# Kernel tuning notes

Measured on AMD Instinct MI355X. Metric: run time of the kernel, lower is better.

The kernel has to match this reference:

```python
import jax, jax.numpy as jnp
import numpy as np

B, L, T, D, H, DH = 8, 1024, 1024, 768, 12, 64
SPATIAL_DIM = 5


def setup_inputs() -> dict:
    key = jax.random.key(0)
    ks = jax.random.split(key, 12)
    scale = 1.0 / np.sqrt(D)
    inp = {
        "q": jax.random.normal(ks[0], (B, L, D), dtype=jnp.float32),
        "k": jax.random.normal(ks[1], (B, T, D), dtype=jnp.float32),
        "v": jax.random.normal(ks[2], (B, T, D), dtype=jnp.float32),
        "pairwise_locs": jax.random.normal(ks[3], (B, L, T, SPATIAL_DIM), dtype=jnp.float32),
        # last 64 key positions are padding in every batch row (never all-True)
        "key_padding_mask": jnp.broadcast_to(jnp.arange(T) >= T - 64, (B, T)),
        "Wq": jax.random.normal(ks[4], (D, H * DH), dtype=jnp.float32) * scale,
        "bq": jnp.zeros((H * DH,), dtype=jnp.float32),
        "Wk": jax.random.normal(ks[5], (D, H * DH), dtype=jnp.float32) * scale,
        "bk": jnp.zeros((H * DH,), dtype=jnp.float32),
        "Wv": jax.random.normal(ks[6], (D, H * DH), dtype=jnp.float32) * scale,
        "bv": jnp.zeros((H * DH,), dtype=jnp.float32),
        "Wo": jax.random.normal(ks[7], (H * DH, D), dtype=jnp.float32) * scale,
        "bo": jnp.zeros((D,), dtype=jnp.float32),
    }
    return inp


def reference(q, k, v, pairwise_locs, key_padding_mask, Wq, bq, Wk, bk, Wv, bv, Wo, bo):
    # pairwise_locs is accepted but unused in this forward path (as in the source).
    b, l, _ = q.shape
    t = k.shape[1]
    qh = (q @ Wq + bq).reshape(b, l, H, DH)  # b l h d
    kh = (k @ Wk + bk).reshape(b, t, H, DH)  # b t h d
    vh = (v @ Wv + bv).reshape(b, t, H, DH)  # b t h d
    attn = jnp.einsum('blhd,bthd->bhlt', qh, kh) / jnp.sqrt(jnp.float32(DH))
    attn = jnp.where(key_padding_mask[:, None, None, :], -jnp.inf, attn)
    fused_attn = jax.nn.softmax(attn, axis=-1)
    out = jnp.einsum('bhlt,bthd->blhd', fused_attn, vh).reshape(b, l, H * DH)
    return out @ Wo + bo  # dropout is identity in eval mode
```

## Files before the change

### kernel.cpp

```cpp
#include <hip/hip_runtime.h>
#include <hip/hip_bf16.h>
#include <cstdint>
#include <cstddef>

#define NB 8
#define NL 1024
#define NT 1024
#define ND 768
#define NH 12
#define NDH 64
#define NM (NB*NL)

typedef short short8 __attribute__((ext_vector_type(8)));
typedef unsigned short ushort4v __attribute__((ext_vector_type(4)));
typedef unsigned int uint4v __attribute__((ext_vector_type(4)));
typedef float f32x4 __attribute__((ext_vector_type(4)));
typedef float float4v __attribute__((ext_vector_type(4)));

__device__ __forceinline__ unsigned short f2bf(float f) {
  union { __hip_bfloat16 h; unsigned short u; } cv;
  cv.h = __float2bfloat16(f);
  return cv.u;
}
__device__ __forceinline__ unsigned pk2(float lo, float hi) {
  return (unsigned)f2bf(lo) | ((unsigned)f2bf(hi) << 16);
}
__device__ __forceinline__ void gll16(const void* g, void* l) {
  __builtin_amdgcn_global_load_lds(
      (const __attribute__((address_space(1))) unsigned int*)g,
      (__attribute__((address_space(3))) unsigned int*)l, 16, 0, 0);
}

__global__ __launch_bounds__(256) void wt_kernel(
    const float* __restrict__ W0, const float* __restrict__ W1,
    const float* __restrict__ W2, const float* __restrict__ W3,
    unsigned short* __restrict__ Wt) {
  __shared__ float tile[32][33];
  const float* W = blockIdx.z == 0 ? W0 : blockIdx.z == 1 ? W1 : blockIdx.z == 2 ? W2 : W3;
  const int k0 = blockIdx.x * 32, n0 = blockIdx.y * 32;
  const int tx = threadIdx.x & 31, ty = threadIdx.x >> 5;
  for (int r = ty; r < 32; r += 8) tile[r][tx] = W[(size_t)(k0 + r) * ND + n0 + tx];
  __syncthreads();
  unsigned short* out = Wt + (size_t)blockIdx.z * ND * ND;
  for (int r = ty; r < 32; r += 8) out[(size_t)(n0 + r) * ND + k0 + tx] = f2bf(tile[tx][r]);
}

template<int PROJ>
__global__ __launch_bounds__(256) void gemm_kernel(
    const float* __restrict__ qf, const float* __restrict__ kf,
    const float* __restrict__ vf, const unsigned short* __restrict__ aob,
    const unsigned short* __restrict__ Wt,
    const float* __restrict__ b0, const float* __restrict__ b1,
    const float* __restrict__ b2, const float* __restrict__ b3,
    unsigned short* __restrict__ qhb, unsigned short* __restrict__ khb,
    unsigned short* __restrict__ vhT, float* __restrict__ outf) {
  __shared__ __align__(16) unsigned short As[128 * 64];
  __shared__ __align__(16) unsigned short Bs[128 * 64];
  const int tid = threadIdx.x, lane = tid & 63, w = tid >> 6;
  const int c = lane & 15, g = lane >> 4;
  const int wrow = w & 1, wcol = w >> 1;
  const int l8 = lane >> 3, l7 = lane & 7, csw = l7 ^ l8;
  const int mbase = blockIdx.x * 128, nbase = blockIdx.y * 128;
  const int z = PROJ ? blockIdx.z : 3;

  const float* Af = PROJ ? (z == 0 ? qf : z == 1 ? kf : vf) : nullptr;
  const unsigned short* Bt = Wt + (size_t)z * ND * ND;
  const float* bias = z == 0 ? b0 : z == 1 ? b1 : z == 2 ? b2 : b3;

  f32x4 acc[4][4];
#pragma unroll
  for (int m = 0; m < 4; m++)
#pragma unroll
    for (int n = 0; n < 4; n++) acc[m][n] = (f32x4){0.f, 0.f, 0.f, 0.f};

  for (int k0 = 0; k0 < ND; k0 += 64) {
    if (PROJ) {
#pragma unroll
      for (int i = 0; i < 4; i++) {
        int id = i * 256 + tid;
        int r = id >> 3, cc = id & 7;
        const float* src = &Af[(size_t)(mbase + r) * ND + k0 + cc * 8];
        float4v x0 = *(const float4v*)src;
        float4v x1 = *(const float4v*)(src + 4);
        uint4v y = {pk2(x0[0], x0[1]), pk2(x0[2], x0[3]),
                    pk2(x1[0], x1[1]), pk2(x1[2], x1[3])};
        *(uint4v*)&As[r * 64 + ((cc ^ (r & 7)) * 8)] = y;
      }
    } else {
#pragma unroll
      for (int it = 0; it < 4; it++) {
        int r = it * 32 + w * 8 + l8;
        gll16(&aob[(size_t)(mbase + r) * ND + k0 + csw * 8],
              &As[(it * 32 + w * 8) * 64]);
      }
    }
#pragma unroll
    for (int it = 0; it < 4; it++) {
      int r = it * 32 + w * 8 + l8;
      gll16(&Bt[(size_t)(nbase + r) * ND + k0 + csw * 8],
            &Bs[(it * 32 + w * 8) * 64]);
    }
    __syncthreads();

#pragma unroll
    for (int ks = 0; ks < 2; ks++) {
      short8 a[4], b[4];
#pragma unroll
      for (int m = 0; m < 4; m++) {
        int r = wrow * 64 + m * 16 + c;
        a[m] = *(const short8*)&As[r * 64 + (((ks * 4 + g) ^ (c & 7)) * 8)];
      }
#pragma unroll
      for (int n = 0; n < 4; n++) {
        int r = wcol * 64 + n * 16 + c;
        b[n] = *(const short8*)&Bs[r * 64 + (((ks * 4 + g) ^ (c & 7)) * 8)];
      }
#pragma unroll
      for (int m = 0; m < 4; m++)
#pragma unroll
        for (int n = 0; n < 4; n++)
          acc[m][n] = __builtin_amdgcn_mfma_f32_16x16x32_bf16(a[m], b[n], acc[m][n], 0, 0, 0);
    }
    __syncthreads();
  }

#pragma unroll
  for (int n = 0; n < 4; n++) {
    const int col = nbase + wcol * 64 + n * 16 + c;
    const float bv = bias[col];
    if (!PROJ) {
#pragma unroll
      for (int m = 0; m < 4; m++) {
        const int r0 = mbase + wrow * 64 + m * 16 + g * 4;
#pragma unroll
        for (int j = 0; j < 4; j++)
          outf[(size_t)(r0 + j) * ND + col] = acc[m][n][j] + bv;
      }
    } else if (z == 2) {
      const int h = col >> 6, dd = col & 63;
#pragma unroll
      for (int m = 0; m < 4; m++) {
        const int r0 = mbase + wrow * 64 + m * 16 + g * 4;
        const int bb = r0 >> 10, t = r0 & (NT - 1);
        ushort4v y;
#pragma unroll
        for (int j = 0; j < 4; j++) y[j] = f2bf(acc[m][n][j] + bv);
        *(ushort4v*)&vhT[((size_t)(bb * NH + h) * NDH + dd) * NT + t] = y;
      }
    } else {
      unsigned short* outb = (z == 0) ? qhb : khb;
      const float scale = (z == 0) ? 0.125f : 1.0f;
#pragma unroll
      for (int m = 0; m < 4; m++) {
        const int r0 = mbase + wrow * 64 + m * 16 + g * 4;
#pragma unroll
        for (int j = 0; j < 4; j++)
          outb[(size_t)(r0 + j) * ND + col] = f2bf((acc[m][n][j] + bv) * scale);
      }
    }
  }
}

__global__ __launch_bounds__(256) void attn_kernel(
    const unsigned short* __restrict__ qh, const unsigned short* __restrict__ kh,
    const unsigned short* __restrict__ vhT, const unsigned int* __restrict__ mask,
    unsigned short* __restrict__ ao) {
  __shared__ __align__(16) unsigned short Ks[2][64 * 64];
  __shared__ __align__(16) unsigned short Vs[2][64 * 64];
  __shared__ __align__(16) unsigned short Ps[4][32][72];
  const int tid = threadIdx.x, lane = tid & 63, w = tid >> 6;
  const int c = lane & 15, g = lane >> 4;
  const int l8 = lane >> 3, l7 = lane & 7, csw = l7 ^ l8;
  const int qb = blockIdx.x * 128;
  const int b = blockIdx.y / NH, h = blockIdx.y % NH;
  const size_t kbase = (size_t)b * NT * ND + h * NDH;
  const size_t vbase = (size_t)(b * NH + h) * NDH * NT;

  short8 aq[2][2];
#pragma unroll
  for (int half = 0; half < 2; half++) {
    size_t qrow = (size_t)(b * NL + qb + w * 32 + half * 16 + c) * ND + h * NDH;
#pragma unroll
    for (int ks = 0; ks < 2; ks++)
      aq[half][ks] = *(const short8*)&qh[qrow + ks * 32 + g * 8];
  }

  f32x4 o[2][4];
#pragma unroll
  for (int half = 0; half < 2; half++)
#pragma unroll
    for (int f = 0; f < 4; f++) o[half][f] = (f32x4){0.f, 0.f, 0.f, 0.f};
  float mr[2] = {-1e30f, -1e30f}, lr[2] = {0.f, 0.f};

#pragma unroll
  for (int it = 0; it < 2; it++) {
    int r = w * 16 + it * 8 + l8;
    gll16(&kh[kbase + (size_t)r * ND + csw * 8], &Ks[0][(w * 16 + it * 8) * 64]);
    gll16(&vhT[vbase + (size_t)r * NT + csw * 8], &Vs[0][(w * 16 + it * 8) * 64]);
  }
  __syncthreads();

  for (int t0 = 0; t0 < NT; t0 += 64) {
    const int cur = (t0 >> 6) & 1;
    if (t0 + 64 < NT) {
#pragma unroll
      for (int it = 0; it < 2; it++) {
        int r = w * 16 + it * 8 + l8;
        gll16(&kh[kbase + (size_t)(t0 + 64 + r) * ND + csw * 8],
              &Ks[cur ^ 1][(w * 16 + it * 8) * 64]);
        gll16(&vhT[vbase + (size_t)r * NT + (t0 + 64) + csw * 8],
              &Vs[cur ^ 1][(w * 16 + it * 8) * 64]);
      }
    }

    f32x4 s[2][4];
#pragma unroll
    for (int half = 0; half < 2; half++)
#pragma unroll
      for (int n = 0; n < 4; n++) s[half][n] = (f32x4){0.f, 0.f, 0.f, 0.f};
#pragma unroll
    for (int ks = 0; ks < 2; ks++)
#pragma unroll
      for (int n = 0; n < 4; n++) {
        short8 ak = *(const short8*)&Ks[cur][(n * 16 + c) * 64 + (((ks * 4 + g) ^ (c & 7)) * 8)];
        s[0][n] = __builtin_amdgcn_mfma_f32_16x16x32_bf16(ak, aq[0][ks], s[0][n], 0, 0, 0);
        s[1][n] = __builtin_amdgcn_mfma_f32_16x16x32_bf16(ak, aq[1][ks], s[1][n], 0, 0, 0);
      }

#pragma unroll
    for (int n = 0; n < 4; n++) {
      uint4v mm = *(const uint4v*)&mask[(size_t)b * NT + t0 + n * 16 + g * 4];
#pragma unroll
      for (int j = 0; j < 4; j++)
        if (mm[j]) { s[0][n][j] = -INFINITY; s[1][n][j] = -INFINITY; }
    }

#pragma unroll
    for (int half = 0; half < 2; half++) {
      float m01 = fmaxf(fmaxf(s[half][0][0], s[half][0][1]), fmaxf(s[half][0][2], s[half][0][3]));
      float m23 = fmaxf(fmaxf(s[half][1][0], s[half][1][1]), fmaxf(s[half][1][2], s[half][1][3]));
      float m45 = fmaxf(fmaxf(s[half][2][0], s[half][2][1]), fmaxf(s[half][2][2], s[half][2][3]));
      float m67 = fmaxf(fmaxf(s[half][3][0], s[half][3][1]), fmaxf(s[half][3][2], s[half][3][3]));
      float mt = fmaxf(fmaxf(m01, m23), fmaxf(m45, m67));
      mt = fmaxf(mt, __shfl_xor(mt, 16, 64));
      mt = fmaxf(mt, __shfl_xor(mt, 32, 64));
      float mnew = fmaxf(mr[half], mt);
      float alpha = __expf(mr[half] - mnew);
      mr[half] = mnew;
      float rs = 0.f;
#pragma unroll
      for (int n = 0; n < 4; n++)
#pragma unroll
        for (int j = 0; j < 4; j++) {
          float p = __expf(s[half][n][j] - mnew);
          s[half][n][j] = p;
          rs += p;
        }
      rs += __shfl_xor(rs, 16, 64);
      rs += __shfl_xor(rs, 32, 64);
      lr[half] = lr[half] * alpha + rs;
#pragma unroll
      for (int f = 0; f < 4; f++)
#pragma unroll
        for (int j = 0; j < 4; j++) o[half][f][j] *= alpha;
      unsigned* pr = (unsigned*)&Ps[w][half * 16 + c][0];
#pragma unroll
      for (int n = 0; n < 4; n++) {
        pr[n * 8 + g * 2]     = pk2(s[half][n][0], s[half][n][1]);
        pr[n * 8 + g * 2 + 1] = pk2(s[half][n][2], s[half][n][3]);
      }
    }

#pragma unroll
    for (int ks = 0; ks < 2; ks++) {
      short8 bp0 = *(const short8*)&Ps[w][c][ks * 32 + g * 8];
      short8 bp1 = *(const short8*)&Ps[w][16 + c][ks * 32 + g * 8];
#pragma unroll
      for (int f = 0; f < 4; f++) {
        short8 av = *(const short8*)&Vs[cur][(f * 16 + c) * 64 + (((ks * 4 + g) ^ (c & 7)) * 8)];
        o[0][f] = __builtin_amdgcn_mfma_f32_16x16x32_bf16(av, bp0, o[0][f], 0, 0, 0);
        o[1][f] = __builtin_amdgcn_mfma_f32_16x16x32_bf16(av, bp1, o[1][f], 0, 0, 0);
      }
    }
    __syncthreads();
  }

#pragma unroll
  for (int half = 0; half < 2; half++) {
    float inv = 1.f / lr[half];
    size_t row = (size_t)(b * NL + qb + w * 32 + half * 16 + c) * ND + h * NDH;
#pragma unroll
    for (int f = 0; f < 4; f++) {
      ushort4v y;
#pragma unroll
      for (int j = 0; j < 4; j++) y[j] = f2bf(o[half][f][j] * inv);
      *(ushort4v*)&ao[row + f * 16 + g * 4] = y;
    }
  }
}

extern "C" void kernel_launch(void* const* d_in, const int* in_sizes, int n_in,
                              void* d_out, int out_size, void* d_ws, size_t ws_size,
                              hipStream_t stream) {
  const float* q  = (const float*)d_in[0];
  const float* k  = (const float*)d_in[1];
  const float* v  = (const float*)d_in[2];
  const unsigned int* mask = (const unsigned int*)d_in[4];
  const float* Wq = (const float*)d_in[5];
  const float* bq = (const float*)d_in[6];
  const float* Wk = (const float*)d_in[7];
  const float* bk = (const float*)d_in[8];
  const float* Wv = (const float*)d_in[9];
  const float* bv = (const float*)d_in[10];
  const float* Wo = (const float*)d_in[11];
  const float* bo = (const float*)d_in[12];
  float* out = (float*)d_out;

  unsigned short* ws  = (unsigned short*)d_ws;
  unsigned short* Wt  = ws;
  unsigned short* qhb = Wt + (size_t)4 * ND * ND;
  unsigned short* khb = qhb + (size_t)NM * ND;
  unsigned short* vhT = khb + (size_t)NM * ND;
  unsigned short* aob = vhT + (size_t)NM * ND;

  wt_kernel<<<dim3(ND / 32, ND / 32, 4), 256, 0, stream>>>(Wq, Wk, Wv, Wo, Wt);

  gemm_kernel<1><<<dim3(NM / 128, ND / 128, 3), 256, 0, stream>>>(
      q, k, v, nullptr, Wt, bq, bk, bv, bo, qhb, khb, vhT, nullptr);

  attn_kernel<<<dim3(NL / 128, NB * NH), 256, 0, stream>>>(qhb, khb, vhT, mask, aob);

  gemm_kernel<0><<<dim3(NM / 128, ND / 128, 1), 256, 0, stream>>>(
      nullptr, nullptr, nullptr, aob, Wt, bq, bk, bv, bo, nullptr, nullptr, nullptr, out);
}
```

Before: 160.6 us.

## Pre-convert inputs to bf16, vectorize GEMM epilogues, add lazy softmax rescale

Adds a separate kernel that converts q/k/v to bf16 up front, so every GEMM stages A through global_load_lds instead of doing per-tile fp32 loads and converts. The GEMM swaps MFMA operand order for non-V modes so each lane holds four consecutive columns, which allows vectorized bias loads and 4-wide stores. The V projection gets its own launch. In attention, the change adds s_setprio around the MFMA blocks, skips masking when a 64-key tile has no padded keys, and only rescales the running max and accumulators when the new max exceeds the old one by more than 8. The cost is an extra launch and an extra bf16 round trip through memory for the inputs. The lazy rescale trades strict max tracking for a bounded exp growth (up to e^8) in fp32.

```diff
diff --git a/kernel.cpp b/kernel.cpp
--- a/kernel.cpp
+++ b/kernel.cpp
@@ -29,6 +29,20 @@
   __builtin_amdgcn_global_load_lds(
       (const __attribute__((address_space(1))) unsigned int*)g,
       (__attribute__((address_space(3))) unsigned int*)l, 16, 0, 0);
+}
+
+__global__ __launch_bounds__(256) void cvt_kernel(
+    const float* __restrict__ q, const float* __restrict__ k,
+    const float* __restrict__ v, unsigned short* __restrict__ qb,
+    unsigned short* __restrict__ kb, unsigned short* __restrict__ vb) {
+  const float* src = blockIdx.y == 0 ? q : blockIdx.y == 1 ? k : v;
+  unsigned short* dst = blockIdx.y == 0 ? qb : blockIdx.y == 1 ? kb : vb;
+  size_t i = ((size_t)blockIdx.x * 256 + threadIdx.x) * 8;
+  float4v x0 = *(const float4v*)&src[i];
+  float4v x1 = *(const float4v*)&src[i + 4];
+  uint4v y = {pk2(x0[0], x0[1]), pk2(x0[2], x0[3]),
+              pk2(x1[0], x1[1]), pk2(x1[2], x1[3])};
+  *(uint4v*)&dst[i] = y;
 }
 
 __global__ __launch_bounds__(256) void wt_kernel(
@@ -45,15 +59,13 @@
   for (int r = ty; r < 32; r += 8) out[(size_t)(n0 + r) * ND + k0 + tx] = f2bf(tile[tx][r]);
 }
 
-template<int PROJ>
+template<int MODE>
 __global__ __launch_bounds__(256) void gemm_kernel(
-    const float* __restrict__ qf, const float* __restrict__ kf,
-    const float* __restrict__ vf, const unsigned short* __restrict__ aob,
+    const unsigned short* __restrict__ A0, const unsigned short* __restrict__ A1,
     const unsigned short* __restrict__ Wt,
-    const float* __restrict__ b0, const float* __restrict__ b1,
-    const float* __restrict__ b2, const float* __restrict__ b3,
-    unsigned short* __restrict__ qhb, unsigned short* __restrict__ khb,
-    unsigned short* __restrict__ vhT, float* __restrict__ outf) {
+    const float* __restrict__ bias0, const float* __restrict__ bias1,
+    unsigned short* __restrict__ outb0, unsigned short* __restrict__ outb1,
+    float* __restrict__ outf) {
   __shared__ __align__(16) unsigned short As[128 * 64];
   __shared__ __align__(16) unsigned short Bs[128 * 64];
   const int tid = threadIdx.x, lane = tid & 63, w = tid >> 6;
@@ -61,11 +73,11 @@
   const int wrow = w & 1, wcol = w >> 1;
   const int l8 = lane >> 3, l7 = lane & 7, csw = l7 ^ l8;
   const int mbase = blockIdx.x * 128, nbase = blockIdx.y * 128;
-  const int z = PROJ ? blockIdx.z : 3;
-
-  const float* Af = PROJ ? (z == 0 ? qf : z == 1 ? kf : vf) : nullptr;
+  const int z = (MODE == 0) ? blockIdx.z : MODE;
+
+  const unsigned short* A = (MODE == 0) ? (z == 0 ? A0 : A1) : A0;
   const unsigned short* Bt = Wt + (size_t)z * ND * ND;
-  const float* bias = z == 0 ? b0 : z == 1 ? b1 : z == 2 ? b2 : b3;
+  const float* bias = (MODE == 0) ? (z == 0 ? bias0 : bias1) : bias0;
 
   f32x4 acc[4][4];
 #pragma unroll
@@ -74,31 +86,11 @@
     for (int n = 0; n < 4; n++) acc[m][n] = (f32x4){0.f, 0.f, 0.f, 0.f};
 
   for (int k0 = 0; k0 < ND; k0 += 64) {
-    if (PROJ) {
-#pragma unroll
-      for (int i = 0; i < 4; i++) {
-        int id = i * 256 + tid;
-        int r = id >> 3, cc = id & 7;
-        const float* src = &Af[(size_t)(mbase + r) * ND + k0 + cc * 8];
-        float4v x0 = *(const float4v*)src;
-        float4v x1 = *(const float4v*)(src + 4);
-        uint4v y = {pk2(x0[0], x0[1]), pk2(x0[2], x0[3]),
-                    pk2(x1[0], x1[1]), pk2(x1[2], x1[3])};
-        *(uint4v*)&As[r * 64 + ((cc ^ (r & 7)) * 8)] = y;
-      }
-    } else {
-#pragma unroll
-      for (int it = 0; it < 4; it++) {
-        int r = it * 32 + w * 8 + l8;
-        gll16(&aob[(size_t)(mbase + r) * ND + k0 + csw * 8],
-              &As[(it * 32 + w * 8) * 64]);
-      }
-    }
 #pragma unroll
     for (int it = 0; it < 4; it++) {
       int r = it * 32 + w * 8 + l8;
-      gll16(&Bt[(size_t)(nbase + r) * ND + k0 + csw * 8],
-            &Bs[(it * 32 + w * 8) * 64]);
+      gll16(&A[(size_t)(mbase + r) * ND + k0 + csw * 8], &As[(it * 32 + w * 8) * 64]);
+      gll16(&Bt[(size_t)(nbase + r) * ND + k0 + csw * 8], &Bs[(it * 32 + w * 8) * 64]);
     }
     __syncthreads();
 
@@ -118,25 +110,21 @@
 #pragma unroll
       for (int m = 0; m < 4; m++)
 #pragma unroll
-        for (int n = 0; n < 4; n++)
-          acc[m][n] = __builtin_amdgcn_mfma_f32_16x16x32_bf16(a[m], b[n], acc[m][n], 0, 0, 0);
+        for (int n = 0; n < 4; n++) {
+          if (MODE == 2)
+            acc[m][n] = __builtin_amdgcn_mfma_f32_16x16x32_bf16(a[m], b[n], acc[m][n], 0, 0, 0);
+          else
+            acc[m][n] = __builtin_amdgcn_mfma_f32_16x16x32_bf16(b[n], a[m], acc[m][n], 0, 0, 0);
+        }
     }
     __syncthreads();
   }
 
-#pragma unroll
-  for (int n = 0; n < 4; n++) {
-    const int col = nbase + wcol * 64 + n * 16 + c;
-    const float bv = bias[col];
-    if (!PROJ) {
-#pragma unroll
-      for (int m = 0; m < 4; m++) {
-        const int r0 = mbase + wrow * 64 + m * 16 + g * 4;
-#pragma unroll
-        for (int j = 0; j < 4; j++)
-          outf[(size_t)(r0 + j) * ND + col] = acc[m][n][j] + bv;
-      }
-    } else if (z == 2) {
+  if (MODE == 2) {
+#pragma unroll
+    for (int n = 0; n < 4; n++) {
+      const int col = nbase + wcol * 64 + n * 16 + c;
+      const float bv = bias[col];
       const int h = col >> 6, dd = col & 63;
 #pragma unroll
       for (int m = 0; m < 4; m++) {
@@ -145,17 +133,30 @@
         ushort4v y;
 #pragma unroll
         for (int j = 0; j < 4; j++) y[j] = f2bf(acc[m][n][j] + bv);
-        *(ushort4v*)&vhT[((size_t)(bb * NH + h) * NDH + dd) * NT + t] = y;
-      }
-    } else {
-      unsigned short* outb = (z == 0) ? qhb : khb;
-      const float scale = (z == 0) ? 0.125f : 1.0f;
+        *(ushort4v*)&outb0[((size_t)(bb * NH + h) * NDH + dd) * NT + t] = y;
+      }
+    }
+  } else {
+    const float scale = (MODE == 0 && z == 0) ? 0.125f : 1.0f;
+    unsigned short* outb = (MODE == 0) ? (z == 0 ? outb0 : outb1) : nullptr;
+#pragma unroll
+    for (int n = 0; n < 4; n++) {
+      const int colb = nbase + wcol * 64 + n * 16 + g * 4;
+      float4v bv4 = *(const float4v*)&bias[colb];
 #pragma unroll
       for (int m = 0; m < 4; m++) {
-        const int r0 = mbase + wrow * 64 + m * 16 + g * 4;
-#pragma unroll
-        for (int j = 0; j < 4; j++)
-          outb[(size_t)(r0 + j) * ND + col] = f2bf((acc[m][n][j] + bv) * scale);
+        const int row = mbase + wrow * 64 + m * 16 + c;
+        if (MODE == 3) {
+          float4v y;
+#pragma unroll
+          for (int j = 0; j < 4; j++) y[j] = acc[m][n][j] + bv4[j];
+          *(float4v*)&outf[(size_t)row * ND + colb] = y;
+        } else {
+          ushort4v y;
+#pragma unroll
+          for (int j = 0; j < 4; j++) y[j] = f2bf((acc[m][n][j] + bv4[j]) * scale);
+          *(ushort4v*)&outb[(size_t)row * ND + colb] = y;
+        }
       }
     }
   }
@@ -218,6 +219,7 @@
     for (int half = 0; half < 2; half++)
 #pragma unroll
       for (int n = 0; n < 4; n++) s[half][n] = (f32x4){0.f, 0.f, 0.f, 0.f};
+    __builtin_amdgcn_s_setprio(1);
 #pragma unroll
     for (int ks = 0; ks < 2; ks++)
 #pragma unroll
@@ -226,13 +228,23 @@
         s[0][n] = __builtin_amdgcn_mfma_f32_16x16x32_bf16(ak, aq[0][ks], s[0][n], 0, 0, 0);
         s[1][n] = __builtin_amdgcn_mfma_f32_16x16x32_bf16(ak, aq[1][ks], s[1][n], 0, 0, 0);
       }
-
-#pragma unroll
-    for (int n = 0; n < 4; n++) {
-      uint4v mm = *(const uint4v*)&mask[(size_t)b * NT + t0 + n * 16 + g * 4];
-#pragma unroll
-      for (int j = 0; j < 4; j++)
-        if (mm[j]) { s[0][n][j] = -INFINITY; s[1][n][j] = -INFINITY; }
+    __builtin_amdgcn_s_setprio(0);
+
+    {
+      uint4v mm[4];
+      unsigned any = 0;
+#pragma unroll
+      for (int n = 0; n < 4; n++) {
+        mm[n] = *(const uint4v*)&mask[(size_t)b * NT + t0 + n * 16 + g * 4];
+        any |= mm[n][0] | mm[n][1] | mm[n][2] | mm[n][3];
+      }
+      if (__any(any != 0u)) {
+#pragma unroll
+        for (int n = 0; n < 4; n++)
+#pragma unroll
+          for (int j = 0; j < 4; j++)
+            if (mm[n][j]) { s[0][n][j] = -INFINITY; s[1][n][j] = -INFINITY; }
+      }
     }
 
 #pragma unroll
@@ -244,25 +256,28 @@
       float mt = fmaxf(fmaxf(m01, m23), fmaxf(m45, m67));
       mt = fmaxf(mt, __shfl_xor(mt, 16, 64));
       mt = fmaxf(mt, __shfl_xor(mt, 32, 64));
-      float mnew = fmaxf(mr[half], mt);
-      float alpha = __expf(mr[half] - mnew);
-      mr[half] = mnew;
+      if (!__all(mt <= mr[half] + 8.f)) {
+        float mnew = fmaxf(mr[half], mt);
+        float alpha = __expf(mr[half] - mnew);
+        lr[half] *= alpha;
+#pragma unroll
+        for (int f = 0; f < 4; f++)
+#pragma unroll
+          for (int j = 0; j < 4; j++) o[half][f][j] *= alpha;
+        mr[half] = mnew;
+      }
       float rs = 0.f;
 #pragma unroll
       for (int n = 0; n < 4; n++)
 #pragma unroll
         for (int j = 0; j < 4; j++) {
-          float p = __expf(s[half][n][j] - mnew);
+          float p = __expf(s[half][n][j] - mr[half]);
           s[half][n][j] = p;
           rs += p;
         }
       rs += __shfl_xor(rs, 16, 64);
       rs += __shfl_xor(rs, 32, 64);
-      lr[half] = lr[half] * alpha + rs;
-#pragma unroll
-      for (int f = 0; f < 4; f++)
-#pragma unroll
-        for (int j = 0; j < 4; j++) o[half][f][j] *= alpha;
+      lr[half] += rs;
       unsigned* pr = (unsigned*)&Ps[w][half * 16 + c][0];
 #pragma unroll
       for (int n = 0; n < 4; n++) {
@@ -271,6 +286,7 @@
       }
     }
 
+    __builtin_amdgcn_s_setprio(1);
 #pragma unroll
     for (int ks = 0; ks < 2; ks++) {
       short8 bp0 = *(const short8*)&Ps[w][c][ks * 32 + g * 8];
@@ -282,6 +298,7 @@
         o[1][f] = __builtin_amdgcn_mfma_f32_16x16x32_bf16(av, bp1, o[1][f], 0, 0, 0);
       }
     }
+    __builtin_amdgcn_s_setprio(0);
     __syncthreads();
   }
 
@@ -318,18 +335,24 @@
 
   unsigned short* ws  = (unsigned short*)d_ws;
   unsigned short* Wt  = ws;
-  unsigned short* qhb = Wt + (size_t)4 * ND * ND;
+  unsigned short* qb  = Wt + (size_t)4 * ND * ND;
+  unsigned short* kb  = qb + (size_t)NM * ND;
+  unsigned short* vb  = kb + (size_t)NM * ND;
+  unsigned short* qhb = vb + (size_t)NM * ND;
   unsigned short* khb = qhb + (size_t)NM * ND;
   unsigned short* vhT = khb + (size_t)NM * ND;
   unsigned short* aob = vhT + (size_t)NM * ND;
 
   wt_kernel<<<dim3(ND / 32, ND / 32, 4), 256, 0, stream>>>(Wq, Wk, Wv, Wo, Wt);
-
-  gemm_kernel<1><<<dim3(NM / 128, ND / 128, 3), 256, 0, stream>>>(
-      q, k, v, nullptr, Wt, bq, bk, bv, bo, qhb, khb, vhT, nullptr);
+  cvt_kernel<<<dim3(NM * ND / 8 / 256, 3), 256, 0, stream>>>(q, k, v, qb, kb, vb);
+
+  gemm_kernel<0><<<dim3(NM / 128, ND / 128, 2), 256, 0, stream>>>(
+      qb, kb, Wt, bq, bk, qhb, khb, nullptr);
+  gemm_kernel<2><<<dim3(NM / 128, ND / 128), 256, 0, stream>>>(
+      vb, nullptr, Wt, bv, nullptr, vhT, nullptr, nullptr);
 
   attn_kernel<<<dim3(NL / 128, NB * NH), 256, 0, stream>>>(qhb, khb, vhT, mask, aob);
 
-  gemm_kernel<0><<<dim3(NM / 128, ND / 128, 1), 256, 0, stream>>>(
-      nullptr, nullptr, nullptr, aob, Wt, bq, bk, bv, bo, nullptr, nullptr, nullptr, out);
-}
+  gemm_kernel<3><<<dim3(NM / 128, ND / 128), 256, 0, stream>>>(
+      aob, nullptr, Wt, bo, nullptr, nullptr, nullptr, out);
+}
```

Measured after the change: 168.9 us. 1.05x slower.
